# Performance work log

Hardware: AMD Instinct MI355X
Metric: run time of the kernel (lower is better)

The kernel has to match this reference:

```python
import jax, jax.numpy as jnp
import numpy as np

M, K, N = 8192, 4096, 4096

def setup_inputs() -> dict:
    key = jax.random.key(0)
    k1, k2, k3, k4, k5 = jax.random.split(key, 5)
    # int8-range quantized tensors stored as int32 (int8 values in [-128, 127])
    inp = jax.random.randint(k1, (M, K), -128, 128, dtype=jnp.int32)
    weight = jax.random.randint(k2, (N, K), -128, 128, dtype=jnp.int32)
    bias = jax.random.normal(k3, (N,), dtype=jnp.float32)
    inp_scales = jax.random.uniform(k4, (1,), jnp.float32, 0.01, 0.05)        # per-tensor
    inp_zero_points = jnp.zeros((1,), jnp.int32)                               # symmetric
    weight_scales = jax.random.uniform(k5, (N,), jnp.float32, 0.005, 0.02)     # per-channel
    weight_zero_points = jnp.zeros((N,), jnp.int32)
    return {
        "inp": inp, "weight": weight, "bias": bias,
        "inp_scales": inp_scales, "inp_zero_points": inp_zero_points,
        "weight_scales": weight_scales, "weight_zero_points": weight_zero_points,
    }

def reference(inp, weight, bias, inp_scales, inp_zero_points, weight_scales, weight_zero_points):
    # qdq_linear fallback path: dequantize activation (per-tensor) and weight
    # (per-output-channel), fp32 matmul, add bias. output_dtype=float32,
    # output_scales/zero_points=None => no output requantization.
    x = (inp.astype(jnp.float32) - inp_zero_points.astype(jnp.float32)) * inp_scales  # [M,K]
    w = (weight.astype(jnp.float32) - weight_zero_points[:, None].astype(jnp.float32)) \
        * weight_scales[:, None]                                                      # [N,K]
    return jnp.einsum('mk,nk->mn', x, w) + bias                                       # [M,N]
```

## Files before the change

### kernel.cpp

```cpp
#include <hip/hip_runtime.h>

#define MM 8192
#define NN 4096
#define KK 4096

#define BM 256
#define BN 256
#define BK 64
#define NT (KK / BK)
#define SLOT_BYTES 32768
#define B_OFF 16384

typedef int int32x4  __attribute__((ext_vector_type(4)));
typedef int int32x16 __attribute__((ext_vector_type(16)));

__device__ __forceinline__ void async_load16(const void* g, void* l) {
  __builtin_amdgcn_global_load_lds(
      (__attribute__((address_space(1))) void*)(void*)g,
      (__attribute__((address_space(3))) void*)l,
      16, 0, 0);
}

__global__ __launch_bounds__(256) void pack_kernel(
    const int* __restrict__ a, const int* __restrict__ w,
    char* __restrict__ a8, char* __restrict__ w8,
    const int* __restrict__ izp, const int* __restrict__ wzp) {
  const long tid = (long)blockIdx.x * 256 + threadIdx.x;
  const long A_T = (long)MM * KK / 16;

  const int4* src;
  int4* dst;
  int z;
  if (tid < A_T) {
    src = (const int4*)a + tid * 4;
    dst = (int4*)a8 + tid;
    z = izp[0];
  } else {
    const long t = tid - A_T;
    src = (const int4*)w + t * 4;
    dst = (int4*)w8 + t;
    z = wzp[t >> 8];
  }

  int4 v0 = src[0], v1 = src[1], v2 = src[2], v3 = src[3];
  union { char c[16]; int4 q; } u;
  u.c[0]  = (char)(v0.x - z); u.c[1]  = (char)(v0.y - z);
  u.c[2]  = (char)(v0.z - z); u.c[3]  = (char)(v0.w - z);
  u.c[4]  = (char)(v1.x - z); u.c[5]  = (char)(v1.y - z);
  u.c[6]  = (char)(v1.z - z); u.c[7]  = (char)(v1.w - z);
  u.c[8]  = (char)(v2.x - z); u.c[9]  = (char)(v2.y - z);
  u.c[10] = (char)(v2.z - z); u.c[11] = (char)(v2.w - z);
  u.c[12] = (char)(v3.x - z); u.c[13] = (char)(v3.y - z);
  u.c[14] = (char)(v3.z - z); u.c[15] = (char)(v3.w - z);
  *dst = u.q;
}

__global__ __launch_bounds__(512, 2) void qgemm_kernel(
    const char* __restrict__ A8, const char* __restrict__ W8,
    float* __restrict__ out,
    const float* __restrict__ bias,
    const float* __restrict__ is_ptr,
    const float* __restrict__ wscale) {
  __shared__ __attribute__((aligned(16))) char lds[4 * SLOT_BYTES];

  int pid = blockIdx.x;
  pid = (pid & 7) * 64 + (pid >> 3);
  const int bm = pid >> 4;
  const int bn = pid & 15;

  const int tid  = threadIdx.x;
  const int wid  = tid >> 6;
  const int lane = tid & 63;
  const int wm = (wid >> 2) * 128;
  const int wn = (wid & 3) * 64;

  const int srow = lane >> 2;
  const int ssub = (lane & 3) ^ ((lane >> 3) & 3);
  const char* a_src[2];
  const char* b_src[2];
  int c_off[2];
#pragma unroll
  for (int i = 0; i < 2; ++i) {
    const int c = wid + i * 8;
    a_src[i] = A8 + (long)(bm * BM + c * 16 + srow) * KK + ssub * 16;
    b_src[i] = W8 + (long)(bn * BN + c * 16 + srow) * KK + ssub * 16;
    c_off[i] = c * 1024;
  }

#define STAGE_A(I, T) \
  async_load16(a_src[I] + (T) * BK, lds + ((T) & 3) * SLOT_BYTES + c_off[I])
#define STAGE_B(I, T) \
  async_load16(b_src[I] + (T) * BK, lds + ((T) & 3) * SLOT_BYTES + B_OFF + c_off[I])

  const int r31 = lane & 31;
  const int hi  = lane >> 5;
  const int rx  = (r31 >> 1) & 3;
  const int ps0 = ((0 + hi) ^ rx) * 16;
  const int ps1 = ((2 + hi) ^ rx) * 16;
  const int a_row = (wm + r31) * BK;
  const int b_row = (wn + r31) * BK;

  int32x16 acc[4][2];
#pragma unroll
  for (int mi = 0; mi < 4; ++mi)
#pragma unroll
    for (int ni = 0; ni < 2; ++ni) acc[mi][ni] = (int32x16)0;

#pragma unroll
  for (int t0 = 0; t0 < 3; ++t0) {
    STAGE_A(0, t0); STAGE_A(1, t0);
    STAGE_B(0, t0); STAGE_B(1, t0);
  }

#define PHASE(PS, SB, STAGE_STMT)                                            \
  {                                                                          \
    const char* ar_ = lds + (SB) + a_row;                                    \
    const char* br_ = lds + (SB) + B_OFF + b_row;                            \
    int32x4 af0 = *(const int32x4*)(ar_ + 0 * 32 * BK + (PS));               \
    int32x4 af1 = *(const int32x4*)(ar_ + 1 * 32 * BK + (PS));               \
    int32x4 af2 = *(const int32x4*)(ar_ + 2 * 32 * BK + (PS));               \
    int32x4 af3 = *(const int32x4*)(ar_ + 3 * 32 * BK + (PS));               \
    int32x4 bf0 = *(const int32x4*)(br_ + 0 * 32 * BK + (PS));               \
    int32x4 bf1 = *(const int32x4*)(br_ + 1 * 32 * BK + (PS));               \
    STAGE_STMT;                                                              \
    __builtin_amdgcn_s_setprio(1);                                           \
    acc[0][0] = __builtin_amdgcn_mfma_i32_32x32x32_i8(af0, bf0, acc[0][0], 0, 0, 0); \
    acc[0][1] = __builtin_amdgcn_mfma_i32_32x32x32_i8(af0, bf1, acc[0][1], 0, 0, 0); \
    acc[1][0] = __builtin_amdgcn_mfma_i32_32x32x32_i8(af1, bf0, acc[1][0], 0, 0, 0); \
    acc[1][1] = __builtin_amdgcn_mfma_i32_32x32x32_i8(af1, bf1, acc[1][1], 0, 0, 0); \
    acc[2][0] = __builtin_amdgcn_mfma_i32_32x32x32_i8(af2, bf0, acc[2][0], 0, 0, 0); \
    acc[2][1] = __builtin_amdgcn_mfma_i32_32x32x32_i8(af2, bf1, acc[2][1], 0, 0, 0); \
    acc[3][0] = __builtin_amdgcn_mfma_i32_32x32x32_i8(af3, bf0, acc[3][0], 0, 0, 0); \
    acc[3][1] = __builtin_amdgcn_mfma_i32_32x32x32_i8(af3, bf1, acc[3][1], 0, 0, 0); \
    __builtin_amdgcn_s_setprio(0);                                           \
  }

#pragma unroll 4
  for (int t = 0; t < NT; ++t) {
    const int sb = (t & 3) * SLOT_BYTES;
    asm volatile("s_waitcnt vmcnt(8)" ::: "memory");
    __builtin_amdgcn_s_barrier();
    PHASE(ps0, sb, if (t < NT - 3) { STAGE_A(0, t + 3); STAGE_A(1, t + 3); })
    PHASE(ps1, sb, if (t < NT - 3) { STAGE_B(0, t + 3); STAGE_B(1, t + 3); })
  }

  const float is0 = is_ptr[0];
  const int row_base = bm * BM + wm + 4 * hi;
  const int col_base = bn * BN + wn + r31;
#pragma unroll
  for (int ni = 0; ni < 2; ++ni) {
    const int col = col_base + ni * 32;
    const float s = is0 * wscale[col];
    const float b = bias[col];
#pragma unroll
    for (int mi = 0; mi < 4; ++mi) {
      const long rb = (long)(row_base + mi * 32) * NN + col;
#pragma unroll
      for (int r = 0; r < 16; ++r) {
        const int roff = (r & 3) + 8 * (r >> 2);
        out[rb + (long)roff * NN] = (float)acc[mi][ni][r] * s + b;
      }
    }
  }
#undef PHASE
#undef STAGE_A
#undef STAGE_B
}

extern "C" void kernel_launch(void* const* d_in, const int* in_sizes, int n_in,
                              void* d_out, int out_size, void* d_ws, size_t ws_size,
                              hipStream_t stream) {
  const int*   inp    = (const int*)d_in[0];
  const int*   weight = (const int*)d_in[1];
  const float* bias   = (const float*)d_in[2];
  const float* iscale = (const float*)d_in[3];
  const int*   izp    = (const int*)d_in[4];
  const float* wscale = (const float*)d_in[5];
  const int*   wzp    = (const int*)d_in[6];
  float* out = (float*)d_out;

  char* a8 = (char*)d_ws;
  char* w8 = a8 + (size_t)MM * KK;

  pack_kernel<<<12288, 256, 0, stream>>>(inp, weight, a8, w8, izp, wzp);

  qgemm_kernel<<<512, 512, 0, stream>>>(a8, w8, out, bias, iscale, wscale);
}
```

Measured before the change: 404.3 us.

## Double-buffer MFMA operand fragments in registers across K half-steps

Restructures the main loop so LDS fragment reads for the next half-tile are issued before the MFMA cluster for the current half-tile runs. Two register sets (a0/b0 and a1/b1) alternate, and the first fragments are preloaded before the loop. The barrier moves between the two halves, with an explicit lgkmcnt(0) wait and vmcnt(4) instead of a single vmcnt(8) wait at the loop head. The goal is to hide LDS read latency behind MFMA work, at the cost of more VGPR pressure under the 2-blocks-per-CU launch bound and a changed async-load wait schedule.

```diff
diff --git a/kernel.cpp b/kernel.cpp
--- a/kernel.cpp
+++ b/kernel.cpp
@@ -106,42 +106,57 @@
 #pragma unroll
     for (int ni = 0; ni < 2; ++ni) acc[mi][ni] = (int32x16)0;
 
+  int32x4 a0[4], b0[2];
+  int32x4 a1[4], b1[2];
+
+#define READ_FRAGS(AF, BF, SB, PS)                                           \
+  {                                                                          \
+    const char* ar_ = lds + (SB) + a_row;                                    \
+    const char* br_ = lds + (SB) + B_OFF + b_row;                            \
+    AF[0] = *(const int32x4*)(ar_ + 0 * 32 * BK + (PS));                     \
+    AF[1] = *(const int32x4*)(ar_ + 1 * 32 * BK + (PS));                     \
+    AF[2] = *(const int32x4*)(ar_ + 2 * 32 * BK + (PS));                     \
+    AF[3] = *(const int32x4*)(ar_ + 3 * 32 * BK + (PS));                     \
+    BF[0] = *(const int32x4*)(br_ + 0 * 32 * BK + (PS));                     \
+    BF[1] = *(const int32x4*)(br_ + 1 * 32 * BK + (PS));                     \
+  }
+
+#define MFMA_CLUSTER(AF, BF)                                                 \
+  {                                                                          \
+    __builtin_amdgcn_s_setprio(1);                                          \
+    acc[0][0] = __builtin_amdgcn_mfma_i32_32x32x32_i8(AF[0], BF[0], acc[0][0], 0, 0, 0); \
+    acc[0][1] = __builtin_amdgcn_mfma_i32_32x32x32_i8(AF[0], BF[1], acc[0][1], 0, 0, 0); \
+    acc[1][0] = __builtin_amdgcn_mfma_i32_32x32x32_i8(AF[1], BF[0], acc[1][0], 0, 0, 0); \
+    acc[1][1] = __builtin_amdgcn_mfma_i32_32x32x32_i8(AF[1], BF[1], acc[1][1], 0, 0, 0); \
+    acc[2][0] = __builtin_amdgcn_mfma_i32_32x32x32_i8(AF[2], BF[0], acc[2][0], 0, 0, 0); \
+    acc[2][1] = __builtin_amdgcn_mfma_i32_32x32x32_i8(AF[2], BF[1], acc[2][1], 0, 0, 0); \
+    acc[3][0] = __builtin_amdgcn_mfma_i32_32x32x32_i8(AF[3], BF[0], acc[3][0], 0, 0, 0); \
+    acc[3][1] = __builtin_amdgcn_mfma_i32_32x32x32_i8(AF[3], BF[1], acc[3][1], 0, 0, 0); \
+    __builtin_amdgcn_s_setprio(0);                                          \
+  }
+
 #pragma unroll
   for (int t0 = 0; t0 < 3; ++t0) {
     STAGE_A(0, t0); STAGE_A(1, t0);
     STAGE_B(0, t0); STAGE_B(1, t0);
   }
-
-#define PHASE(PS, SB, STAGE_STMT)                                            \
-  {                                                                          \
-    const char* ar_ = lds + (SB) + a_row;                                    \
-    const char* br_ = lds + (SB) + B_OFF + b_row;                            \
-    int32x4 af0 = *(const int32x4*)(ar_ + 0 * 32 * BK + (PS));               \
-    int32x4 af1 = *(const int32x4*)(ar_ + 1 * 32 * BK + (PS));               \
-    int32x4 af2 = *(const int32x4*)(ar_ + 2 * 32 * BK + (PS));               \
-    int32x4 af3 = *(const int32x4*)(ar_ + 3 * 32 * BK + (PS));               \
-    int32x4 bf0 = *(const int32x4*)(br_ + 0 * 32 * BK + (PS));               \
-    int32x4 bf1 = *(const int32x4*)(br_ + 1 * 32 * BK + (PS));               \
-    STAGE_STMT;                                                              \
-    __builtin_amdgcn_s_setprio(1);                                           \
-    acc[0][0] = __builtin_amdgcn_mfma_i32_32x32x32_i8(af0, bf0, acc[0][0], 0, 0, 0); \
-    acc[0][1] = __builtin_amdgcn_mfma_i32_32x32x32_i8(af0, bf1, acc[0][1], 0, 0, 0); \
-    acc[1][0] = __builtin_amdgcn_mfma_i32_32x32x32_i8(af1, bf0, acc[1][0], 0, 0, 0); \
-    acc[1][1] = __builtin_amdgcn_mfma_i32_32x32x32_i8(af1, bf1, acc[1][1], 0, 0, 0); \
-    acc[2][0] = __builtin_amdgcn_mfma_i32_32x32x32_i8(af2, bf0, acc[2][0], 0, 0, 0); \
-    acc[2][1] = __builtin_amdgcn_mfma_i32_32x32x32_i8(af2, bf1, acc[2][1], 0, 0, 0); \
-    acc[3][0] = __builtin_amdgcn_mfma_i32_32x32x32_i8(af3, bf0, acc[3][0], 0, 0, 0); \
-    acc[3][1] = __builtin_amdgcn_mfma_i32_32x32x32_i8(af3, bf1, acc[3][1], 0, 0, 0); \
-    __builtin_amdgcn_s_setprio(0);                                           \
-  }
+  asm volatile("s_waitcnt vmcnt(8)" ::: "memory");
+  __builtin_amdgcn_s_barrier();
+  READ_FRAGS(a0, b0, 0, ps0);
 
 #pragma unroll 4
   for (int t = 0; t < NT; ++t) {
-    const int sb = (t & 3) * SLOT_BYTES;
-    asm volatile("s_waitcnt vmcnt(8)" ::: "memory");
+    const int sb  = (t & 3) * SLOT_BYTES;
+    const int sb1 = ((t + 1) & 3) * SLOT_BYTES;
+    if (t + 3 < NT) { STAGE_A(0, t + 3); STAGE_A(1, t + 3); }
+    READ_FRAGS(a1, b1, sb, ps1);
+    MFMA_CLUSTER(a0, b0);
+    asm volatile("s_waitcnt lgkmcnt(0)" ::: "memory");
+    asm volatile("s_waitcnt vmcnt(4)" ::: "memory");
     __builtin_amdgcn_s_barrier();
-    PHASE(ps0, sb, if (t < NT - 3) { STAGE_A(0, t + 3); STAGE_A(1, t + 3); })
-    PHASE(ps1, sb, if (t < NT - 3) { STAGE_B(0, t + 3); STAGE_B(1, t + 3); })
+    if (t + 3 < NT) { STAGE_B(0, t + 3); STAGE_B(1, t + 3); }
+    READ_FRAGS(a0, b0, sb1, ps0);
+    MFMA_CLUSTER(a1, b1);
   }
 
   const float is0 = is_ptr[0];
@@ -162,7 +177,8 @@
       }
     }
   }
-#undef PHASE
+#undef READ_FRAGS
+#undef MFMA_CLUSTER
 #undef STAGE_A
 #undef STAGE_B
 }
```

Result: no change. 409.8 us (+1.4%).

## Load weight fragments directly from global in MFMA-ready layout, bypass LDS

Applied to the files above, without the earlier changes.

The pack kernel now writes weights in a blocked layout (32 rows by 16-byte k-chunks) so each lane can load its MFMA B fragment straight from global memory into registers, double-buffered across k-tiles. Only A goes through LDS, and BK doubles to 128 so the whole LDS slot holds a larger A tile. A is software-pipelined with register double buffering and a single barrier per tile. The goal is to halve LDS traffic and barrier pressure. The cost is more VGPRs and B reads that rely on L2 rather than shared-memory reuse across waves, and the waitcnt accounting is fragile.

```diff
diff --git a/kernel.cpp b/kernel.cpp
--- a/kernel.cpp
+++ b/kernel.cpp
@@ -6,10 +6,9 @@
 
 #define BM 256
 #define BN 256
-#define BK 64
+#define BK 128
 #define NT (KK / BK)
 #define SLOT_BYTES 32768
-#define B_OFF 16384
 
 typedef int int32x4  __attribute__((ext_vector_type(4)));
 typedef int int32x16 __attribute__((ext_vector_type(16)));
@@ -37,9 +36,14 @@
     z = izp[0];
   } else {
     const long t = tid - A_T;
-    src = (const int4*)w + t * 4;
-    dst = (int4*)w8 + t;
-    z = wzp[t >> 8];
+    const int nb  = (int)(t >> 13);
+    const int rem = (int)(t & 8191);
+    const int kc  = rem >> 5;
+    const int n5  = rem & 31;
+    const int n   = nb * 32 + n5;
+    src = (const int4*)(w + (long)n * KK + kc * 16);
+    dst = (int4*)(w8 + (long)nb * 131072 + kc * 512 + n5 * 16);
+    z = wzp[n];
   }
 
   int4 v0 = src[0], v1 = src[1], v2 = src[2], v3 = src[3];
@@ -74,31 +78,61 @@
   const int wm = (wid >> 2) * 128;
   const int wn = (wid & 3) * 64;
 
-  const int srow = lane >> 2;
-  const int ssub = (lane & 3) ^ ((lane >> 3) & 3);
-  const char* a_src[2];
-  const char* b_src[2];
-  int c_off[2];
-#pragma unroll
-  for (int i = 0; i < 2; ++i) {
+  const int srow = lane >> 3;
+  const int ssub = (lane & 7) ^ srow;
+  const char* a_src[4];
+  int c_off[4];
+#pragma unroll
+  for (int i = 0; i < 4; ++i) {
     const int c = wid + i * 8;
-    a_src[i] = A8 + (long)(bm * BM + c * 16 + srow) * KK + ssub * 16;
-    b_src[i] = W8 + (long)(bn * BN + c * 16 + srow) * KK + ssub * 16;
+    a_src[i] = A8 + (long)(bm * BM + c * 8 + srow) * KK + ssub * 16;
     c_off[i] = c * 1024;
   }
 
-#define STAGE_A(I, T) \
-  async_load16(a_src[I] + (T) * BK, lds + ((T) & 3) * SLOT_BYTES + c_off[I])
-#define STAGE_B(I, T) \
-  async_load16(b_src[I] + (T) * BK, lds + ((T) & 3) * SLOT_BYTES + B_OFF + c_off[I])
+#define STAGE_A4(T)                                                          \
+  {                                                                          \
+    char* sl_ = lds + ((T) & 3) * SLOT_BYTES;                                \
+    async_load16(a_src[0] + (T) * BK, sl_ + c_off[0]);                       \
+    async_load16(a_src[1] + (T) * BK, sl_ + c_off[1]);                       \
+    async_load16(a_src[2] + (T) * BK, sl_ + c_off[2]);                       \
+    async_load16(a_src[3] + (T) * BK, sl_ + c_off[3]);                       \
+  }
 
   const int r31 = lane & 31;
   const int hi  = lane >> 5;
-  const int rx  = (r31 >> 1) & 3;
-  const int ps0 = ((0 + hi) ^ rx) * 16;
-  const int ps1 = ((2 + hi) ^ rx) * 16;
+  const int ps0 = ((0 + hi) ^ (r31 & 7)) * 16;
+  const int ps1 = ((2 + hi) ^ (r31 & 7)) * 16;
+  const int ps2 = ((4 + hi) ^ (r31 & 7)) * 16;
+  const int ps3 = ((6 + hi) ^ (r31 & 7)) * 16;
   const int a_row = (wm + r31) * BK;
-  const int b_row = (wn + r31) * BK;
+
+  const char* b_ptr[2];
+#pragma unroll
+  for (int ni = 0; ni < 2; ++ni) {
+    const int nbg = (bn * BN + wn + ni * 32) >> 5;
+    b_ptr[ni] = W8 + (long)nbg * 131072 + hi * 512 + r31 * 16;
+  }
+
+#define LOAD_B(SET, T)                                                       \
+  {                                                                          \
+    SET[0][0] = *(const int32x4*)(b_ptr[0] + (T) * 4096 + 0 * 1024);         \
+    SET[0][1] = *(const int32x4*)(b_ptr[0] + (T) * 4096 + 1 * 1024);         \
+    SET[0][2] = *(const int32x4*)(b_ptr[0] + (T) * 4096 + 2 * 1024);         \
+    SET[0][3] = *(const int32x4*)(b_ptr[0] + (T) * 4096 + 3 * 1024);         \
+    SET[1][0] = *(const int32x4*)(b_ptr[1] + (T) * 4096 + 0 * 1024);         \
+    SET[1][1] = *(const int32x4*)(b_ptr[1] + (T) * 4096 + 1 * 1024);         \
+    SET[1][2] = *(const int32x4*)(b_ptr[1] + (T) * 4096 + 2 * 1024);         \
+    SET[1][3] = *(const int32x4*)(b_ptr[1] + (T) * 4096 + 3 * 1024);         \
+  }
+
+#define READ_A(DST, T, PS)                                                   \
+  {                                                                          \
+    const char* ar_ = lds + ((T) & 3) * SLOT_BYTES + a_row;                  \
+    DST[0] = *(const int32x4*)(ar_ + 0 * 4096 + (PS));                       \
+    DST[1] = *(const int32x4*)(ar_ + 1 * 4096 + (PS));                       \
+    DST[2] = *(const int32x4*)(ar_ + 2 * 4096 + (PS));                       \
+    DST[3] = *(const int32x4*)(ar_ + 3 * 4096 + (PS));                       \
+  }
 
   int32x16 acc[4][2];
 #pragma unroll
@@ -106,42 +140,51 @@
 #pragma unroll
     for (int ni = 0; ni < 2; ++ni) acc[mi][ni] = (int32x16)0;
 
-#pragma unroll
-  for (int t0 = 0; t0 < 3; ++t0) {
-    STAGE_A(0, t0); STAGE_A(1, t0);
-    STAGE_B(0, t0); STAGE_B(1, t0);
-  }
-
-#define PHASE(PS, SB, STAGE_STMT)                                            \
-  {                                                                          \
-    const char* ar_ = lds + (SB) + a_row;                                    \
-    const char* br_ = lds + (SB) + B_OFF + b_row;                            \
-    int32x4 af0 = *(const int32x4*)(ar_ + 0 * 32 * BK + (PS));               \
-    int32x4 af1 = *(const int32x4*)(ar_ + 1 * 32 * BK + (PS));               \
-    int32x4 af2 = *(const int32x4*)(ar_ + 2 * 32 * BK + (PS));               \
-    int32x4 af3 = *(const int32x4*)(ar_ + 3 * 32 * BK + (PS));               \
-    int32x4 bf0 = *(const int32x4*)(br_ + 0 * 32 * BK + (PS));               \
-    int32x4 bf1 = *(const int32x4*)(br_ + 1 * 32 * BK + (PS));               \
-    STAGE_STMT;                                                              \
+  int32x4 a0[4], a1[4];
+  int32x4 bE[2][4], bO[2][4];
+
+#define MFMA8(AF, BSET, S)                                                   \
+  {                                                                          \
     __builtin_amdgcn_s_setprio(1);                                           \
-    acc[0][0] = __builtin_amdgcn_mfma_i32_32x32x32_i8(af0, bf0, acc[0][0], 0, 0, 0); \
-    acc[0][1] = __builtin_amdgcn_mfma_i32_32x32x32_i8(af0, bf1, acc[0][1], 0, 0, 0); \
-    acc[1][0] = __builtin_amdgcn_mfma_i32_32x32x32_i8(af1, bf0, acc[1][0], 0, 0, 0); \
-    acc[1][1] = __builtin_amdgcn_mfma_i32_32x32x32_i8(af1, bf1, acc[1][1], 0, 0, 0); \
-    acc[2][0] = __builtin_amdgcn_mfma_i32_32x32x32_i8(af2, bf0, acc[2][0], 0, 0, 0); \
-    acc[2][1] = __builtin_amdgcn_mfma_i32_32x32x32_i8(af2, bf1, acc[2][1], 0, 0, 0); \
-    acc[3][0] = __builtin_amdgcn_mfma_i32_32x32x32_i8(af3, bf0, acc[3][0], 0, 0, 0); \
-    acc[3][1] = __builtin_amdgcn_mfma_i32_32x32x32_i8(af3, bf1, acc[3][1], 0, 0, 0); \
+    acc[0][0] = __builtin_amdgcn_mfma_i32_32x32x32_i8(AF[0], BSET[0][S], acc[0][0], 0, 0, 0); \
+    acc[0][1] = __builtin_amdgcn_mfma_i32_32x32x32_i8(AF[0], BSET[1][S], acc[0][1], 0, 0, 0); \
+    acc[1][0] = __builtin_amdgcn_mfma_i32_32x32x32_i8(AF[1], BSET[0][S], acc[1][0], 0, 0, 0); \
+    acc[1][1] = __builtin_amdgcn_mfma_i32_32x32x32_i8(AF[1], BSET[1][S], acc[1][1], 0, 0, 0); \
+    acc[2][0] = __builtin_amdgcn_mfma_i32_32x32x32_i8(AF[2], BSET[0][S], acc[2][0], 0, 0, 0); \
+    acc[2][1] = __builtin_amdgcn_mfma_i32_32x32x32_i8(AF[2], BSET[1][S], acc[2][1], 0, 0, 0); \
+    acc[3][0] = __builtin_amdgcn_mfma_i32_32x32x32_i8(AF[3], BSET[0][S], acc[3][0], 0, 0, 0); \
+    acc[3][1] = __builtin_amdgcn_mfma_i32_32x32x32_i8(AF[3], BSET[1][S], acc[3][1], 0, 0, 0); \
     __builtin_amdgcn_s_setprio(0);                                           \
   }
 
-#pragma unroll 4
-  for (int t = 0; t < NT; ++t) {
-    const int sb = (t & 3) * SLOT_BYTES;
-    asm volatile("s_waitcnt vmcnt(8)" ::: "memory");
-    __builtin_amdgcn_s_barrier();
-    PHASE(ps0, sb, if (t < NT - 3) { STAGE_A(0, t + 3); STAGE_A(1, t + 3); })
-    PHASE(ps1, sb, if (t < NT - 3) { STAGE_B(0, t + 3); STAGE_B(1, t + 3); })
+#define TILE_BODY(T, BCUR, BNXT)                                             \
+  {                                                                          \
+    const int t_ = (T);                                                      \
+    if (t_ + 1 < NT) LOAD_B(BNXT, t_ + 1);                                   \
+    if (t_ + 3 < NT) STAGE_A4(t_ + 3);                                       \
+    READ_A(a1, t_, ps1);                                                     \
+    MFMA8(a0, BCUR, 0);                                                      \
+    READ_A(a0, t_, ps2);                                                     \
+    MFMA8(a1, BCUR, 1);                                                      \
+    READ_A(a1, t_, ps3);                                                     \
+    MFMA8(a0, BCUR, 2);                                                      \
+    asm volatile("s_waitcnt vmcnt(24) lgkmcnt(0)" ::: "memory");             \
+    __builtin_amdgcn_s_barrier();                                            \
+    if (t_ + 1 < NT) READ_A(a0, t_ + 1, ps0);                                \
+    MFMA8(a1, BCUR, 3);                                                      \
+  }
+
+  STAGE_A4(0);
+  STAGE_A4(1);
+  STAGE_A4(2);
+  LOAD_B(bE, 0);
+  asm volatile("s_waitcnt vmcnt(16)" ::: "memory");
+  __builtin_amdgcn_s_barrier();
+  READ_A(a0, 0, ps0);
+
+  for (int u = 0; u < NT / 2; ++u) {
+    TILE_BODY(2 * u,     bE, bO);
+    TILE_BODY(2 * u + 1, bO, bE);
   }
 
   const float is0 = is_ptr[0];
@@ -162,9 +205,11 @@
       }
     }
   }
-#undef PHASE
-#undef STAGE_A
-#undef STAGE_B
+#undef TILE_BODY
+#undef MFMA8
+#undef READ_A
+#undef LOAD_B
+#undef STAGE_A4
 }
 
 extern "C" void kernel_launch(void* const* d_in, const int* in_sizes, int n_in,
```

Measured after the change: 425.8 us. 5.3% more time.

## Restructure int8 GEMM to 128x256 tiles, 4-wave blocks, triple-buffered ping-pong pipeline

Applied to the files above, without the earlier changes.

Changes the GEMM block tile from 256x256 with 8 waves to 128x256 with 4 waves, doubling the grid. The LDS ring drops from four slots to three, and the k-loop is rewritten as explicit fragment-read, async-stage and MFMA phases separated by barriers and sched_barrier. The pack kernel now has each thread handle 4 ints instead of 16. The aim is higher occupancy and better overlap of global-to-LDS loads with MFMA. The cost is lower operand reuse per block, more global traffic for W, and extra barriers.

```diff
diff --git a/kernel.cpp b/kernel.cpp
--- a/kernel.cpp
+++ b/kernel.cpp
@@ -4,12 +4,13 @@
 #define NN 4096
 #define KK 4096
 
-#define BM 256
+#define BM 128
 #define BN 256
 #define BK 64
 #define NT (KK / BK)
-#define SLOT_BYTES 32768
-#define B_OFF 16384
+#define A_BYTES (BM * BK)
+#define B_BYTES (BN * BK)
+#define SLOT (A_BYTES + B_BYTES)
 
 typedef int int32x4  __attribute__((ext_vector_type(4)));
 typedef int int32x16 __attribute__((ext_vector_type(16)));
@@ -26,71 +27,72 @@
     char* __restrict__ a8, char* __restrict__ w8,
     const int* __restrict__ izp, const int* __restrict__ wzp) {
   const long tid = (long)blockIdx.x * 256 + threadIdx.x;
-  const long A_T = (long)MM * KK / 16;
+  const long A_T = (long)MM * KK / 4;
 
   const int4* src;
-  int4* dst;
+  int* dst;
   int z;
   if (tid < A_T) {
-    src = (const int4*)a + tid * 4;
-    dst = (int4*)a8 + tid;
+    src = (const int4*)a + tid;
+    dst = (int*)a8 + tid;
     z = izp[0];
   } else {
-    const long t = tid - A_T;
-    src = (const int4*)w + t * 4;
-    dst = (int4*)w8 + t;
-    z = wzp[t >> 8];
-  }
-
-  int4 v0 = src[0], v1 = src[1], v2 = src[2], v3 = src[3];
-  union { char c[16]; int4 q; } u;
-  u.c[0]  = (char)(v0.x - z); u.c[1]  = (char)(v0.y - z);
-  u.c[2]  = (char)(v0.z - z); u.c[3]  = (char)(v0.w - z);
-  u.c[4]  = (char)(v1.x - z); u.c[5]  = (char)(v1.y - z);
-  u.c[6]  = (char)(v1.z - z); u.c[7]  = (char)(v1.w - z);
-  u.c[8]  = (char)(v2.x - z); u.c[9]  = (char)(v2.y - z);
-  u.c[10] = (char)(v2.z - z); u.c[11] = (char)(v2.w - z);
-  u.c[12] = (char)(v3.x - z); u.c[13] = (char)(v3.y - z);
-  u.c[14] = (char)(v3.z - z); u.c[15] = (char)(v3.w - z);
+    long t = tid - A_T;
+    src = (const int4*)w + t;
+    dst = (int*)w8 + t;
+    z = wzp[t >> 10];
+  }
+
+  int4 v = *src;
+  union { char c[4]; int q; } u;
+  u.c[0] = (char)(v.x - z);
+  u.c[1] = (char)(v.y - z);
+  u.c[2] = (char)(v.z - z);
+  u.c[3] = (char)(v.w - z);
   *dst = u.q;
 }
 
-__global__ __launch_bounds__(512, 2) void qgemm_kernel(
+__global__ __launch_bounds__(256, 2) void qgemm_kernel(
     const char* __restrict__ A8, const char* __restrict__ W8,
     float* __restrict__ out,
     const float* __restrict__ bias,
     const float* __restrict__ is_ptr,
     const float* __restrict__ wscale) {
-  __shared__ __attribute__((aligned(16))) char lds[4 * SLOT_BYTES];
+  __shared__ __attribute__((aligned(16))) char lds[3 * SLOT];
 
   int pid = blockIdx.x;
-  pid = (pid & 7) * 64 + (pid >> 3);
+  pid = (pid & 7) * 128 + (pid >> 3);
   const int bm = pid >> 4;
   const int bn = pid & 15;
 
   const int tid  = threadIdx.x;
   const int wid  = tid >> 6;
   const int lane = tid & 63;
-  const int wm = (wid >> 2) * 128;
-  const int wn = (wid & 3) * 64;
+  const int wm = (wid & 1) * 64;
+  const int wn = (wid >> 1) * 128;
 
   const int srow = lane >> 2;
   const int ssub = (lane & 3) ^ ((lane >> 3) & 3);
   const char* a_src[2];
-  const char* b_src[2];
-  int c_off[2];
+  const char* b_src[4];
+  int a_off[2], b_off[4];
 #pragma unroll
   for (int i = 0; i < 2; ++i) {
-    const int c = wid + i * 8;
+    const int c = wid + i * 4;
     a_src[i] = A8 + (long)(bm * BM + c * 16 + srow) * KK + ssub * 16;
-    b_src[i] = W8 + (long)(bn * BN + c * 16 + srow) * KK + ssub * 16;
-    c_off[i] = c * 1024;
-  }
-
-#define STAGE_A(I, T) \
-  async_load16(a_src[I] + (T) * BK, lds + ((T) & 3) * SLOT_BYTES + c_off[I])
-#define STAGE_B(I, T) \
-  async_load16(b_src[I] + (T) * BK, lds + ((T) & 3) * SLOT_BYTES + B_OFF + c_off[I])
+    a_off[i] = c * 1024;
+  }
+#pragma unroll
+  for (int j = 0; j < 4; ++j) {
+    const int c = wid + j * 4;
+    b_src[j] = W8 + (long)(bn * BN + c * 16 + srow) * KK + ssub * 16;
+    b_off[j] = c * 1024;
+  }
+
+#define STAGE_A(I, T, SS) \
+  async_load16(a_src[I] + (T) * BK, lds + (SS) + a_off[I])
+#define STAGE_B(J, T, SS) \
+  async_load16(b_src[J] + (T) * BK, lds + (SS) + A_BYTES + b_off[J])
 
   const int r31 = lane & 31;
   const int hi  = lane >> 5;
@@ -100,60 +102,102 @@
   const int a_row = (wm + r31) * BK;
   const int b_row = (wn + r31) * BK;
 
-  int32x16 acc[4][2];
-#pragma unroll
-  for (int mi = 0; mi < 4; ++mi)
-#pragma unroll
-    for (int ni = 0; ni < 2; ++ni) acc[mi][ni] = (int32x16)0;
-
-#pragma unroll
-  for (int t0 = 0; t0 < 3; ++t0) {
-    STAGE_A(0, t0); STAGE_A(1, t0);
-    STAGE_B(0, t0); STAGE_B(1, t0);
-  }
-
-#define PHASE(PS, SB, STAGE_STMT)                                            \
-  {                                                                          \
-    const char* ar_ = lds + (SB) + a_row;                                    \
-    const char* br_ = lds + (SB) + B_OFF + b_row;                            \
-    int32x4 af0 = *(const int32x4*)(ar_ + 0 * 32 * BK + (PS));               \
-    int32x4 af1 = *(const int32x4*)(ar_ + 1 * 32 * BK + (PS));               \
-    int32x4 af2 = *(const int32x4*)(ar_ + 2 * 32 * BK + (PS));               \
-    int32x4 af3 = *(const int32x4*)(ar_ + 3 * 32 * BK + (PS));               \
-    int32x4 bf0 = *(const int32x4*)(br_ + 0 * 32 * BK + (PS));               \
-    int32x4 bf1 = *(const int32x4*)(br_ + 1 * 32 * BK + (PS));               \
-    STAGE_STMT;                                                              \
+  int32x16 acc[2][4];
+#pragma unroll
+  for (int mi = 0; mi < 2; ++mi)
+#pragma unroll
+    for (int ni = 0; ni < 4; ++ni) acc[mi][ni] = (int32x16)0;
+
+  int32x4 af0, af1, bf0, bf1, bf2, bf3;
+
+#define READ_FRAGS(SR, PS)                                                   \
+  {                                                                          \
+    const char* ar_ = lds + (SR) + a_row;                                    \
+    const char* br_ = lds + (SR) + A_BYTES + b_row;                          \
+    af0 = *(const int32x4*)(ar_ + 0 * 2048 + (PS));                          \
+    af1 = *(const int32x4*)(ar_ + 1 * 2048 + (PS));                          \
+    bf0 = *(const int32x4*)(br_ + 0 * 2048 + (PS));                          \
+    bf1 = *(const int32x4*)(br_ + 1 * 2048 + (PS));                          \
+    bf2 = *(const int32x4*)(br_ + 2 * 2048 + (PS));                          \
+    bf3 = *(const int32x4*)(br_ + 3 * 2048 + (PS));                          \
+  }
+
+#define MFMA_PHASE()                                                         \
+  {                                                                          \
+    __builtin_amdgcn_sched_barrier(0);                                       \
     __builtin_amdgcn_s_setprio(1);                                           \
     acc[0][0] = __builtin_amdgcn_mfma_i32_32x32x32_i8(af0, bf0, acc[0][0], 0, 0, 0); \
     acc[0][1] = __builtin_amdgcn_mfma_i32_32x32x32_i8(af0, bf1, acc[0][1], 0, 0, 0); \
+    acc[0][2] = __builtin_amdgcn_mfma_i32_32x32x32_i8(af0, bf2, acc[0][2], 0, 0, 0); \
+    acc[0][3] = __builtin_amdgcn_mfma_i32_32x32x32_i8(af0, bf3, acc[0][3], 0, 0, 0); \
     acc[1][0] = __builtin_amdgcn_mfma_i32_32x32x32_i8(af1, bf0, acc[1][0], 0, 0, 0); \
     acc[1][1] = __builtin_amdgcn_mfma_i32_32x32x32_i8(af1, bf1, acc[1][1], 0, 0, 0); \
-    acc[2][0] = __builtin_amdgcn_mfma_i32_32x32x32_i8(af2, bf0, acc[2][0], 0, 0, 0); \
-    acc[2][1] = __builtin_amdgcn_mfma_i32_32x32x32_i8(af2, bf1, acc[2][1], 0, 0, 0); \
-    acc[3][0] = __builtin_amdgcn_mfma_i32_32x32x32_i8(af3, bf0, acc[3][0], 0, 0, 0); \
-    acc[3][1] = __builtin_amdgcn_mfma_i32_32x32x32_i8(af3, bf1, acc[3][1], 0, 0, 0); \
+    acc[1][2] = __builtin_amdgcn_mfma_i32_32x32x32_i8(af1, bf2, acc[1][2], 0, 0, 0); \
+    acc[1][3] = __builtin_amdgcn_mfma_i32_32x32x32_i8(af1, bf3, acc[1][3], 0, 0, 0); \
     __builtin_amdgcn_s_setprio(0);                                           \
   }
 
-#pragma unroll 4
-  for (int t = 0; t < NT; ++t) {
-    const int sb = (t & 3) * SLOT_BYTES;
-    asm volatile("s_waitcnt vmcnt(8)" ::: "memory");
-    __builtin_amdgcn_s_barrier();
-    PHASE(ps0, sb, if (t < NT - 3) { STAGE_A(0, t + 3); STAGE_A(1, t + 3); })
-    PHASE(ps1, sb, if (t < NT - 3) { STAGE_B(0, t + 3); STAGE_B(1, t + 3); })
-  }
+#define TILE_FULL(T, SR, SS)                                                 \
+  {                                                                          \
+     \
+    READ_FRAGS(SR, ps0);                                                     \
+    STAGE_A(0, (T) + 2, SS); STAGE_A(1, (T) + 2, SS);                        \
+    STAGE_B(0, (T) + 2, SS);                                                 \
+    __builtin_amdgcn_s_barrier();                                            \
+    MFMA_PHASE();                                                            \
+    __builtin_amdgcn_s_barrier();                                            \
+      \
+    READ_FRAGS(SR, ps1);                                                     \
+    STAGE_B(1, (T) + 2, SS); STAGE_B(2, (T) + 2, SS);                        \
+    STAGE_B(3, (T) + 2, SS);                                                 \
+    asm volatile("s_waitcnt vmcnt(6)" ::: "memory");                         \
+    __builtin_amdgcn_s_barrier();                                            \
+    MFMA_PHASE();                                                            \
+    __builtin_amdgcn_s_barrier();                                            \
+  }
+
+#define TILE_TAIL(SR)                                                        \
+  {                                                                          \
+    READ_FRAGS(SR, ps0);                                                     \
+    __builtin_amdgcn_s_barrier();                                            \
+    MFMA_PHASE();                                                            \
+    __builtin_amdgcn_s_barrier();                                            \
+    READ_FRAGS(SR, ps1);                                                     \
+    __builtin_amdgcn_s_barrier();                                            \
+    MFMA_PHASE();                                                            \
+    __builtin_amdgcn_s_barrier();                                            \
+  }
+
+  STAGE_A(0, 0, 0); STAGE_A(1, 0, 0);
+  STAGE_B(0, 0, 0); STAGE_B(1, 0, 0); STAGE_B(2, 0, 0); STAGE_B(3, 0, 0);
+  STAGE_A(0, 1, SLOT); STAGE_A(1, 1, SLOT);
+  STAGE_B(0, 1, SLOT); STAGE_B(1, 1, SLOT);
+  STAGE_B(2, 1, SLOT); STAGE_B(3, 1, SLOT);
+  asm volatile("s_waitcnt vmcnt(6)" ::: "memory");
+  __builtin_amdgcn_s_barrier();
+
+  for (int u = 0; u < 60; u += 3) {
+    TILE_FULL(u + 0, 0 * SLOT, 2 * SLOT);
+    TILE_FULL(u + 1, 1 * SLOT, 0 * SLOT);
+    TILE_FULL(u + 2, 2 * SLOT, 1 * SLOT);
+  }
+  TILE_FULL(60, 0 * SLOT, 2 * SLOT);
+  TILE_FULL(61, 1 * SLOT, 0 * SLOT);
+  asm volatile("s_waitcnt vmcnt(0)" ::: "memory");
+  __builtin_amdgcn_s_barrier();
+  TILE_TAIL(2 * SLOT);
+  TILE_TAIL(0 * SLOT);
 
   const float is0 = is_ptr[0];
   const int row_base = bm * BM + wm + 4 * hi;
   const int col_base = bn * BN + wn + r31;
 #pragma unroll
-  for (int ni = 0; ni < 2; ++ni) {
+  for (int ni = 0; ni < 4; ++ni) {
     const int col = col_base + ni * 32;
     const float s = is0 * wscale[col];
     const float b = bias[col];
 #pragma unroll
-    for (int mi = 0; mi < 4; ++mi) {
+    for (int mi = 0; mi < 2; ++mi) {
       const long rb = (long)(row_base + mi * 32) * NN + col;
 #pragma unroll
       for (int r = 0; r < 16; ++r) {
@@ -162,7 +206,10 @@
       }
     }
   }
-#undef PHASE
+#undef TILE_TAIL
+#undef TILE_FULL
+#undef MFMA_PHASE
+#undef READ_FRAGS
 #undef STAGE_A
 #undef STAGE_B
 }
@@ -182,7 +229,7 @@
   char* a8 = (char*)d_ws;
   char* w8 = a8 + (size_t)MM * KK;
 
-  pack_kernel<<<12288, 256, 0, stream>>>(inp, weight, a8, w8, izp, wzp);
-
-  qgemm_kernel<<<512, 512, 0, stream>>>(a8, w8, out, bias, iscale, wscale);
-}
+  pack_kernel<<<49152, 256, 0, stream>>>(inp, weight, a8, w8, izp, wzp);
+
+  qgemm_kernel<<<1024, 256, 0, stream>>>(a8, w8, out, bias, iscale, wscale);
+}
```

Result: slower. 413.6 us (+2.3%).
